# Kernel optimization log

Measured on AMD Instinct MI355X. Metric: run time of the kernel, lower is better.

## Reference

```python
import jax, jax.numpy as jnp
import numpy as np


def _log_g(x):
    # log of g(x) = where(x>=0, x+0.5, sigmoid(x)), computed stably in log-space
    return jnp.where(x >= 0, jnp.log(jax.nn.relu(x) + 0.5), -jax.nn.softplus(-x))


def _mingru_layer(h, w_hg_l, w_out_l, rms_w_l):
    # h: [B,T,H]; w_hg_l: [2*DI,H]; w_out_l: [H,DI]; rms_w_l: [H]
    hg = jnp.einsum('bth,dh->btd', h, w_hg_l)          # [B,T,2*DI]
    hidden, gate = jnp.split(hg, 2, axis=-1)            # each [B,T,DI]
    log_coeffs = -jax.nn.softplus(gate)                 # log a_t
    log_values = -jax.nn.softplus(-gate) + _log_g(hidden)  # log(z_t * g(h~_t))
    # Heinsen log-space associative scan (prev_hidden = 0, contributes nothing)
    a_star = jnp.cumsum(log_coeffs, axis=1)
    log_h = a_star + jax.lax.cumlogsumexp(log_values - a_star, axis=1)
    out = jnp.exp(log_h)                                # [B,T,DI]
    out = jnp.einsum('btd,hd->bth', out, w_out_l) + h   # proj_out + residual
    eps = jnp.finfo(out.dtype).eps
    out = out * jax.lax.rsqrt(jnp.mean(out * out, axis=-1, keepdims=True) + eps)
    return out * rms_w_l


def setup_inputs() -> dict:
    key = jax.random.key(0)
    ks = jax.random.split(key, 6)
    B, T, OBS, H, DI, L, A = 32, 1024, 512, 512, 1024, 2, 16
    s = 0.05  # weight scale keeps softplus/exp chain well-conditioned
    return {
        'x': jax.random.normal(ks[0], (B, T, OBS), jnp.float32),
        'enc_w': s * jax.random.normal(ks[1], (H, OBS), jnp.float32),
        'enc_b': jnp.zeros((H,), jnp.float32),
        'w_hg': s * jax.random.normal(ks[2], (L, 2 * DI, H), jnp.float32),
        'w_out': s * jax.random.normal(ks[3], (L, H, DI), jnp.float32),
        'rms_w': jnp.ones((L, H), jnp.float32),
        'dec_w': s * jax.random.normal(ks[4], (A, H), jnp.float32),
        'dec_b': jnp.zeros((A,), jnp.float32),
        'val_w': s * jax.random.normal(ks[5], (1, H), jnp.float32),
        'val_b': jnp.zeros((1,), jnp.float32),
    }


def reference(x, enc_w, enc_b, w_hg, w_out, rms_w, dec_w, dec_b, val_w, val_b):
    B, T, _ = x.shape
    # encoder: Linear + exact gelu
    h = jax.nn.gelu(jnp.einsum('bto,ho->bth', x, enc_w) + enc_b, approximate=False)
    for l in range(w_hg.shape[0]):
        h = _mingru_layer(h, w_hg[l], w_out[l], rms_w[l])
    flat = h.reshape(B * T, -1)
    logits = flat @ dec_w.T + dec_b                     # [B*T, A]
    values = (flat @ val_w.T + val_b).reshape(B, T)
    return logits, values
```

## Files before the change

### kernel.cpp

```cpp
#include <hip/hip_runtime.h>
#include <math.h>

#define MROWS 32768
#define T_LEN 1024

typedef __attribute__((ext_vector_type(8))) short bf16x8;
typedef __attribute__((ext_vector_type(4))) float f32x4;

__device__ __forceinline__ unsigned short f2bf(float f) {
  union { float f; unsigned u; } x; x.f = f;
  unsigned r = x.u + 0x7fffu + ((x.u >> 16) & 1u);
  return (unsigned short)(r >> 16);
}
__device__ __forceinline__ float bf2f(unsigned short u) {
  union { unsigned u; float f; } x; x.u = ((unsigned)u) << 16; return x.f;
}

__device__ __forceinline__ void gload_lds16(const void* g, void* l) {
  __builtin_amdgcn_global_load_lds(
      (const __attribute__((address_space(1))) void*)g,
      (__attribute__((address_space(3))) void*)l, 16, 0, 0);
}

__device__ __forceinline__ float sigm_neg(float x) {
  return __builtin_amdgcn_rcpf(1.0f + __expf(x));
}

#define VMCNT2 asm volatile("s_waitcnt vmcnt(2)" ::: "memory")
#define VMCNT0 asm volatile("s_waitcnt vmcnt(0)" ::: "memory")
#define LGKM0 do { asm volatile("s_waitcnt lgkmcnt(0)" ::: "memory"); \
                   __builtin_amdgcn_sched_barrier(0); } while (0)
#define BAR __builtin_amdgcn_s_barrier()

template<int MODE>
__global__ __launch_bounds__(256, 2)
void gemm_bt(const unsigned short* __restrict__ A, int lda,
             const unsigned short* __restrict__ B,
             int N, int K,
             const float* __restrict__ bias,
             const unsigned short* res,
             unsigned short* outb)
{
  __shared__ __align__(16) unsigned short sA[128 * 64];
  __shared__ __align__(16) unsigned short sB[128 * 64];
  const int tid  = threadIdx.x;
  const int wave = tid >> 6, lane = tid & 63;
  const int lid = blockIdx.x;
  const int swz = (lid & 7) * ((int)gridDim.x >> 3) + (lid >> 3);
  const int m0 = (swz >> 2) * 128;
  const int n0 = (swz & 3) * 128;
  const int srow   = lane >> 3;
  const int sslotb = ((lane & 7) ^ srow) * 16;
  const int wm = wave & 1, wn = wave >> 1;
  const int r16 = lane & 15, q = lane >> 4;

  f32x4 acc[4][4];
#pragma unroll
  for (int i = 0; i < 4; i++)
#pragma unroll
    for (int j = 0; j < 4; j++)
#pragma unroll
      for (int e = 0; e < 4; e++) acc[i][j][e] = 0.0f;

  const char* Ab = (const char*)A;
  const char* Bb = (const char*)B;
  char* sAb = (char*)sA;
  char* sBb = (char*)sB;

  for (int kt = 0; kt < K; kt += 64) {
#pragma unroll
    for (int i = 0; i < 4; i++) {
      const int j = wave * 4 + i;
      const int row = j * 8 + srow;
      gload_lds16(Ab + ((size_t)(m0 + row) * lda + kt) * 2 + sslotb, sAb + j * 1024);
      gload_lds16(Bb + ((size_t)(n0 + row) * K   + kt) * 2 + sslotb, sBb + j * 1024);
    }
    __syncthreads();
#pragma unroll
    for (int kh = 0; kh < 2; kh++) {
      bf16x8 af[4], bfr[4];
#pragma unroll
      for (int mt = 0; mt < 4; mt++) {
        const int row = wm * 64 + mt * 16 + r16;
        af[mt] = *(const bf16x8*)(sAb + row * 128 + ((((kh << 2) | q) ^ (row & 7)) * 16));
      }
#pragma unroll
      for (int nt = 0; nt < 4; nt++) {
        const int row = wn * 64 + nt * 16 + r16;
        bfr[nt] = *(const bf16x8*)(sBb + row * 128 + ((((kh << 2) | q) ^ (row & 7)) * 16));
      }
#pragma unroll
      for (int mt = 0; mt < 4; mt++)
#pragma unroll
        for (int nt = 0; nt < 4; nt++)
          acc[mt][nt] = __builtin_amdgcn_mfma_f32_16x16x32_bf16(af[mt], bfr[nt], acc[mt][nt], 0, 0, 0);
    }
    __syncthreads();
  }

#pragma unroll
  for (int mt = 0; mt < 4; mt++) {
#pragma unroll
    for (int nt = 0; nt < 4; nt++) {
#pragma unroll
      for (int r = 0; r < 4; r++) {
        const int m = m0 + wm * 64 + mt * 16 + q * 4 + r;
        const int n = n0 + wn * 64 + nt * 16 + r16;
        const size_t idx = (size_t)m * N + n;
        float v = acc[mt][nt][r];
        if (MODE == 0) {
          v += bias[n];
          v = 0.5f * v * (1.0f + erff(v * 0.70710678118654752f));
        } else if (MODE == 2) {
          v += bf2f(res[idx]);
        }
        outb[idx] = f2bf(v);
      }
    }
  }
}

__global__ __launch_bounds__(512, 2)
void gemm_hg8(const unsigned short* __restrict__ A,
              const unsigned short* __restrict__ B,
              unsigned short* __restrict__ outb)
{
  __shared__ __align__(16) char smem[131072];
  const int tid  = threadIdx.x;
  const int wave = tid >> 6, lane = tid & 63;
  const int lid = blockIdx.x;
  const int swz = (lid & 7) * 128 + (lid >> 3);
  const int m0  = (swz >> 3) * 256;
  const int nh0 = (swz & 7) * 128;
  const int wm = wave >> 2, wn = wave & 3;
  const int r16 = lane & 15, q4 = lane >> 4;

  const int srow   = tid >> 3;
  const int sslotb = ((tid & 7) ^ (srow & 7)) * 16;
  const int sldso  = tid * 16;

  const int slot0 = ((q4)     ^ (r16 & 7)) * 16;
  const int slot1 = ((4 | q4) ^ (r16 & 7)) * 16;

  const char* Ab = (const char*)A;
  const char* Bb = (const char*)B;

  f32x4 acc[8][4];
#pragma unroll
  for (int i = 0; i < 8; i++)
#pragma unroll
    for (int j = 0; j < 4; j++)
#pragma unroll
      for (int e = 0; e < 4; e++) acc[i][j][e] = 0.0f;

  auto stage2 = [&](int u, int qp) {
    char* base = smem + (u & 1) * 65536;
    const int kt2 = u << 7;
#pragma unroll
    for (int i = 0; i < 2; ++i) {
      const int qq = qp * 2 + i;
      if (qq < 4) {
        gload_lds16(Ab + (size_t)(m0 + qq * 64 + srow) * 1024 + kt2 + sslotb,
                    base + qq * 8192 + sldso);
      } else if (qq < 6) {
        gload_lds16(Bb + (size_t)(nh0 + (qq - 4) * 64 + srow) * 1024 + kt2 + sslotb,
                    base + 32768 + (qq - 4) * 8192 + sldso);
      } else {
        gload_lds16(Bb + (size_t)(1024 + nh0 + (qq - 6) * 64 + srow) * 1024 + kt2 + sslotb,
                    base + 49152 + (qq - 6) * 8192 + sldso);
      }
    }
  };

  auto lda_frags = [&](const char* base, int kh, int mh,
                       bf16x8 af[4], bf16x8 bh[2], bf16x8 bg[2]) {
    const int slot = kh ? slot1 : slot0;
#pragma unroll
    for (int mt = 0; mt < 4; ++mt) {
      const int row = wm * 128 + mh * 64 + mt * 16 + r16;
      af[mt] = *(const bf16x8*)(base + row * 128 + slot);
    }
#pragma unroll
    for (int nt = 0; nt < 2; ++nt) {
      const int row = wn * 32 + nt * 16 + r16;
      bh[nt] = *(const bf16x8*)(base + 32768 + row * 128 + slot);
      bg[nt] = *(const bf16x8*)(base + 49152 + row * 128 + slot);
    }
  };

  auto mfma16 = [&](int mh, bf16x8 af[4], bf16x8 bh[2], bf16x8 bg[2]) {
    __builtin_amdgcn_s_setprio(1);
#pragma unroll
    for (int mt = 0; mt < 4; ++mt) {
      const int MT = mh * 4 + mt;
      acc[MT][0] = __builtin_amdgcn_mfma_f32_16x16x32_bf16(af[mt], bh[0], acc[MT][0], 0, 0, 0);
      acc[MT][1] = __builtin_amdgcn_mfma_f32_16x16x32_bf16(af[mt], bh[1], acc[MT][1], 0, 0, 0);
      acc[MT][2] = __builtin_amdgcn_mfma_f32_16x16x32_bf16(af[mt], bg[0], acc[MT][2], 0, 0, 0);
      acc[MT][3] = __builtin_amdgcn_mfma_f32_16x16x32_bf16(af[mt], bg[1], acc[MT][3], 0, 0, 0);
    }
    __builtin_amdgcn_s_setprio(0);
  };

#pragma unroll
  for (int qp = 0; qp < 4; ++qp) stage2(0, qp);
  VMCNT0; BAR;

  for (int t = 0; t < 4; ++t) {
    const int u1 = 2 * t + 1;
    const char* b0 = smem;
    const char* b1 = smem + 65536;
    bf16x8 af[4], bh[2], bg[2];
    const bool more = (t < 3);

#pragma unroll
    for (int pi = 0; pi < 4; ++pi) {
      const int kh = pi >> 1, mh = pi & 1;
      if (pi == 0) {
        stage2(u1, 0);
        VMCNT2;
        BAR;
        lda_frags(b0, kh, mh, af, bh, bg);
      } else {
        lda_frags(b0, kh, mh, af, bh, bg);
        stage2(u1, pi);
        BAR;
      }
      LGKM0;
      mfma16(mh, af, bh, bg);
      BAR;
    }

#pragma unroll
    for (int pi = 0; pi < 4; ++pi) {
      const int kh = pi >> 1, mh = pi & 1;
      if (pi == 0) {
        if (more) { stage2(u1 + 1, 0); VMCNT2; } else { VMCNT0; }
        BAR;
        lda_frags(b1, kh, mh, af, bh, bg);
      } else {
        lda_frags(b1, kh, mh, af, bh, bg);
        if (more) stage2(u1 + 1, pi);
        BAR;
      }
      LGKM0;
      mfma16(mh, af, bh, bg);
      BAR;
    }
  }

#pragma unroll
  for (int MT = 0; MT < 8; ++MT) {
#pragma unroll
    for (int nf = 0; nf < 2; ++nf) {
#pragma unroll
      for (int r = 0; r < 4; ++r) {
        const int m = m0 + wm * 128 + MT * 16 + q4 * 4 + r;
        const int d = nh0 + wn * 32 + nf * 16 + r16;
        const float vh = acc[MT][nf][r];
        const float vg = acc[MT][nf + 2][r];
        const float G = (vh >= 0.0f) ? (vh + 0.5f) : sigm_neg(-vh);
        const float a = sigm_neg(vg);
        const float b = (1.0f - a) * G;
        const size_t base = (size_t)m * 2048 + d;
        outb[base]        = f2bf(b);
        outb[base + 1024] = f2bf(a);
      }
    }
  }
}

__global__ __launch_bounds__(256)
void scan_kernel(unsigned short* hg) {
  __shared__ unsigned long long sAB[256 * 16];
  __shared__ float sA[16 * 32];
  __shared__ float sH[16 * 32];
  const int b  = blockIdx.x >> 5;
  const int dg = blockIdx.x & 31;
  const int tid = threadIdx.x;
  const int c  = tid >> 4;
  const int dp = tid & 15;
  unsigned int* base = (unsigned int*)(hg + (size_t)b * T_LEN * 2048);
  const int du = dg * 16 + dp;

  float carry = 0.0f;

  for (int seg = 0; seg < 4; ++seg) {
    const int t0 = seg * 256 + c * 16;

    float A0 = 1.0f, A1 = 1.0f, h0 = 0.0f, h1 = 0.0f;
#pragma unroll
    for (int tl = 0; tl < 16; ++tl) {
      const int t = t0 + tl;
      const unsigned bpk = base[t * 1024 + du];
      const unsigned apk = base[t * 1024 + 512 + du];
      sAB[(c * 16 + tl) * 16 + dp] =
          (unsigned long long)apk | ((unsigned long long)bpk << 32);
      const float fa0 = bf2f((unsigned short)apk), fa1 = bf2f((unsigned short)(apk >> 16));
      const float fb0 = bf2f((unsigned short)bpk), fb1 = bf2f((unsigned short)(bpk >> 16));
      A0 *= fa0; h0 = fa0 * h0 + fb0;
      A1 *= fa1; h1 = fa1 * h1 + fb1;
    }
    sA[c * 32 + 2 * dp] = A0;  sA[c * 32 + 2 * dp + 1] = A1;
    sH[c * 32 + 2 * dp] = h0;  sH[c * 32 + 2 * dp + 1] = h1;
    __syncthreads();

    if (tid < 32) {
      float hin = carry;
#pragma unroll
      for (int cc = 0; cc < 16; ++cc) {
        const float a  = sA[cc * 32 + tid];
        const float hs = sH[cc * 32 + tid];
        sA[cc * 32 + tid] = hin;
        hin = hs + a * hin;
      }
      carry = hin;
    }
    __syncthreads();

    float hh0 = sA[c * 32 + 2 * dp];
    float hh1 = sA[c * 32 + 2 * dp + 1];
#pragma unroll
    for (int tl = 0; tl < 16; ++tl) {
      const int t = t0 + tl;
      const unsigned long long ab = sAB[(c * 16 + tl) * 16 + dp];
      const float fa0 = bf2f((unsigned short)ab);
      const float fa1 = bf2f((unsigned short)(ab >> 16));
      const float fb0 = bf2f((unsigned short)(ab >> 32));
      const float fb1 = bf2f((unsigned short)(ab >> 48));
      hh0 = fa0 * hh0 + fb0;
      hh1 = fa1 * hh1 + fb1;
      base[t * 1024 + 512 + du] = (unsigned)f2bf(hh0) | ((unsigned)f2bf(hh1) << 16);
    }
    __syncthreads();
  }
}

__global__ __launch_bounds__(256)
void rms_kernel(unsigned short* __restrict__ hb, const float* __restrict__ w) {
  const int wid  = (blockIdx.x * blockDim.x + threadIdx.x) >> 6;
  const int lane = threadIdx.x & 63;
  unsigned short* row = hb + (size_t)wid * 512;
  float v[8];
  float ss = 0.0f;
#pragma unroll
  for (int j = 0; j < 8; j++) { v[j] = bf2f(row[lane + 64 * j]); ss += v[j] * v[j]; }
#pragma unroll
  for (int off = 32; off >= 1; off >>= 1) ss += __shfl_xor(ss, off, 64);
  const float r = rsqrtf(ss * (1.0f / 512.0f) + 1.1920929e-7f);
#pragma unroll
  for (int j = 0; j < 8; j++) {
    const int k = lane + 64 * j;
    row[k] = f2bf(v[j] * r * w[k]);
  }
}

__global__ __launch_bounds__(256)
void rms_dec_kernel(const unsigned short* __restrict__ hb,
                    const float* __restrict__ w,
                    const float* __restrict__ dec_w,
                    const float* __restrict__ dec_b,
                    const float* __restrict__ val_w,
                    const float* __restrict__ val_b,
                    float* __restrict__ out) {
  const int row  = (blockIdx.x * blockDim.x + threadIdx.x) >> 6;
  const int lane = threadIdx.x & 63;
  const unsigned short* hr = hb + (size_t)row * 512;
  float v[8];
  float ss = 0.0f;
#pragma unroll
  for (int j = 0; j < 8; j++) { v[j] = bf2f(hr[lane + 64 * j]); ss += v[j] * v[j]; }
#pragma unroll
  for (int off = 32; off >= 1; off >>= 1) ss += __shfl_xor(ss, off, 64);
  const float r = rsqrtf(ss * (1.0f / 512.0f) + 1.1920929e-7f);

  float acc[17];
#pragma unroll
  for (int a = 0; a < 17; a++) acc[a] = 0.0f;
#pragma unroll
  for (int j = 0; j < 8; j++) {
    const int k = lane + 64 * j;
    const float hv = v[j] * r * w[k];
#pragma unroll
    for (int a = 0; a < 16; a++) acc[a] += hv * dec_w[a * 512 + k];
    acc[16] += hv * val_w[k];
  }
#pragma unroll
  for (int a = 0; a < 17; a++) {
#pragma unroll
    for (int off = 32; off >= 1; off >>= 1) acc[a] += __shfl_xor(acc[a], off, 64);
  }
  if (lane == 0) {
    float* logits = out;
    float* values = out + (size_t)MROWS * 16;
#pragma unroll
    for (int a = 0; a < 16; a++) logits[(size_t)row * 16 + a] = acc[a] + dec_b[a];
    values[row] = acc[16] + val_b[0];
  }
}

__global__ __launch_bounds__(256)
void conv_bf16(const float* __restrict__ in, unsigned short* __restrict__ out, int n4) {
  const int i = blockIdx.x * blockDim.x + threadIdx.x;
  if (i < n4) {
    const float4 v = ((const float4*)in)[i];
    const unsigned long long pack =
        (unsigned long long)f2bf(v.x) |
        ((unsigned long long)f2bf(v.y) << 16) |
        ((unsigned long long)f2bf(v.z) << 32) |
        ((unsigned long long)f2bf(v.w) << 48);
    ((unsigned long long*)out)[i] = pack;
  }
}

extern "C" void kernel_launch(void* const* d_in, const int* in_sizes, int n_in,
                              void* d_out, int out_size, void* d_ws, size_t ws_size,
                              hipStream_t stream) {
  const float* x     = (const float*)d_in[0];
  const float* enc_w = (const float*)d_in[1];
  const float* enc_b = (const float*)d_in[2];
  const float* w_hg  = (const float*)d_in[3];
  const float* w_out = (const float*)d_in[4];
  const float* rms_w = (const float*)d_in[5];
  const float* dec_w = (const float*)d_in[6];
  const float* dec_b = (const float*)d_in[7];
  const float* val_w = (const float*)d_in[8];
  const float* val_b = (const float*)d_in[9];
  float* out = (float*)d_out;

  if (ws_size < 174587904u) return;

  char* ws = (char*)d_ws;
  unsigned short* hg   = (unsigned short*)(ws);
  unsigned short* xb   = (unsigned short*)(ws);
  unsigned short* hb   = (unsigned short*)(ws + 134217728);
  unsigned short* wenc = (unsigned short*)(ws + 167772160);
  unsigned short* whg  = wenc + 262144;
  unsigned short* wout = whg + 2097152;

  conv_bf16<<<16384, 256, 0, stream>>>(x, xb, 4194304);
  conv_bf16<<<256,   256, 0, stream>>>(enc_w, wenc, 65536);
  conv_bf16<<<2048,  256, 0, stream>>>(w_hg, whg, 524288);
  conv_bf16<<<1024,  256, 0, stream>>>(w_out, wout, 262144);

  gemm_bt<0><<<1024, 256, 0, stream>>>(xb, 512, wenc, 512, 512, enc_b, nullptr, hb);

  for (int l = 0; l < 2; ++l) {
    gemm_hg8<<<1024, 512, 0, stream>>>(hb, whg + (size_t)l * 1048576, hg);
    scan_kernel<<<1024, 256, 0, stream>>>(hg);
    gemm_bt<2><<<1024, 256, 0, stream>>>(hg + 1024, 2048, wout + (size_t)l * 524288,
                                         512, 1024, nullptr, hb, hb);
    if (l == 0) rms_kernel<<<8192, 256, 0, stream>>>(hb, rms_w);
  }

  rms_dec_kernel<<<8192, 256, 0, stream>>>(hb, rms_w + 512, dec_w, dec_b,
                                           val_w, val_b, out);
}
```

Measured before the change: 572.5 us.

## Fuse x fp32-to-bf16 conversion into encoder GEMM and load A from global

Removes the standalone conversion pass over the input x. The encoder GEMM now reads fp32 A rows straight from global memory and converts them in registers. The out-projection GEMM also reads A fragments directly from global instead of staging them in LDS, and raises its occupancy hint. The three weight conversions are merged into one launch. The trade-off is less coalesced, unstaged global reads of A (reused across the wn waves only through cache) in place of the shared-memory tiles.

```diff
diff --git a/kernel.cpp b/kernel.cpp
--- a/kernel.cpp
+++ b/kernel.cpp
@@ -20,6 +20,12 @@
   __builtin_amdgcn_global_load_lds(
       (const __attribute__((address_space(1))) void*)g,
       (__attribute__((address_space(3))) void*)l, 16, 0, 0);
+}
+
+__device__ __forceinline__ unsigned cvt_pk_bf16(float lo, float hi) {
+  unsigned r;
+  asm volatile("v_cvt_pk_bf16_f32 %0, %1, %2" : "=v"(r) : "v"(lo), "v"(hi));
+  return r;
 }
 
 __device__ __forceinline__ float sigm_neg(float x) {
@@ -32,16 +38,12 @@
                    __builtin_amdgcn_sched_barrier(0); } while (0)
 #define BAR __builtin_amdgcn_s_barrier()
 
-template<int MODE>
 __global__ __launch_bounds__(256, 2)
-void gemm_bt(const unsigned short* __restrict__ A, int lda,
-             const unsigned short* __restrict__ B,
-             int N, int K,
-             const float* __restrict__ bias,
-             const unsigned short* res,
-             unsigned short* outb)
+void gemm_enc(const float* __restrict__ A,
+              const unsigned short* __restrict__ B,
+              const float* __restrict__ bias,
+              unsigned short* __restrict__ outb)
 {
-  __shared__ __align__(16) unsigned short sA[128 * 64];
   __shared__ __align__(16) unsigned short sB[128 * 64];
   const int tid  = threadIdx.x;
   const int wave = tid >> 6, lane = tid & 63;
@@ -62,18 +64,15 @@
 #pragma unroll
       for (int e = 0; e < 4; e++) acc[i][j][e] = 0.0f;
 
-  const char* Ab = (const char*)A;
   const char* Bb = (const char*)B;
-  char* sAb = (char*)sA;
   char* sBb = (char*)sB;
 
-  for (int kt = 0; kt < K; kt += 64) {
+  for (int kt = 0; kt < 512; kt += 64) {
 #pragma unroll
     for (int i = 0; i < 4; i++) {
       const int j = wave * 4 + i;
       const int row = j * 8 + srow;
-      gload_lds16(Ab + ((size_t)(m0 + row) * lda + kt) * 2 + sslotb, sAb + j * 1024);
-      gload_lds16(Bb + ((size_t)(n0 + row) * K   + kt) * 2 + sslotb, sBb + j * 1024);
+      gload_lds16(Bb + ((size_t)(n0 + row) * 512 + kt) * 2 + sslotb, sBb + j * 1024);
     }
     __syncthreads();
 #pragma unroll
@@ -81,8 +80,16 @@
       bf16x8 af[4], bfr[4];
 #pragma unroll
       for (int mt = 0; mt < 4; mt++) {
-        const int row = wm * 64 + mt * 16 + r16;
-        af[mt] = *(const bf16x8*)(sAb + row * 128 + ((((kh << 2) | q) ^ (row & 7)) * 16));
+        const float* ar = A + (size_t)(m0 + wm * 64 + mt * 16 + r16) * 512
+                            + kt + kh * 32 + q * 8;
+        const float4 x0 = *(const float4*)ar;
+        const float4 x1 = *(const float4*)(ar + 4);
+        union { unsigned u[4]; bf16x8 v; } cv;
+        cv.u[0] = cvt_pk_bf16(x0.x, x0.y);
+        cv.u[1] = cvt_pk_bf16(x0.z, x0.w);
+        cv.u[2] = cvt_pk_bf16(x1.x, x1.y);
+        cv.u[3] = cvt_pk_bf16(x1.z, x1.w);
+        af[mt] = cv.v;
       }
 #pragma unroll
       for (int nt = 0; nt < 4; nt++) {
@@ -106,15 +113,84 @@
       for (int r = 0; r < 4; r++) {
         const int m = m0 + wm * 64 + mt * 16 + q * 4 + r;
         const int n = n0 + wn * 64 + nt * 16 + r16;
-        const size_t idx = (size_t)m * N + n;
-        float v = acc[mt][nt][r];
-        if (MODE == 0) {
-          v += bias[n];
-          v = 0.5f * v * (1.0f + erff(v * 0.70710678118654752f));
-        } else if (MODE == 2) {
-          v += bf2f(res[idx]);
-        }
-        outb[idx] = f2bf(v);
+        float v = acc[mt][nt][r] + bias[n];
+        v = 0.5f * v * (1.0f + erff(v * 0.70710678118654752f));
+        outb[(size_t)m * 512 + n] = f2bf(v);
+      }
+    }
+  }
+}
+
+__global__ __launch_bounds__(256, 4)
+void gemm_oproj(const unsigned short* __restrict__ A,
+                const unsigned short* __restrict__ B,
+                const unsigned short* __restrict__ res,
+                unsigned short* __restrict__ outb)
+{
+  __shared__ __align__(16) unsigned short sB[128 * 64];
+  const int tid  = threadIdx.x;
+  const int wave = tid >> 6, lane = tid & 63;
+  const int lid = blockIdx.x;
+  const int swz = (lid & 7) * ((int)gridDim.x >> 3) + (lid >> 3);
+  const int m0 = (swz >> 2) * 128;
+  const int n0 = (swz & 3) * 128;
+  const int srow   = lane >> 3;
+  const int sslotb = ((lane & 7) ^ srow) * 16;
+  const int wm = wave & 1, wn = wave >> 1;
+  const int r16 = lane & 15, q = lane >> 4;
+
+  f32x4 acc[4][4];
+#pragma unroll
+  for (int i = 0; i < 4; i++)
+#pragma unroll
+    for (int j = 0; j < 4; j++)
+#pragma unroll
+      for (int e = 0; e < 4; e++) acc[i][j][e] = 0.0f;
+
+  const char* Ab = (const char*)A;
+  const char* Bb = (const char*)B;
+  char* sBb = (char*)sB;
+
+  for (int kt = 0; kt < 1024; kt += 64) {
+#pragma unroll
+    for (int i = 0; i < 4; i++) {
+      const int j = wave * 4 + i;
+      const int row = j * 8 + srow;
+      gload_lds16(Bb + ((size_t)(n0 + row) * 1024 + kt) * 2 + sslotb, sBb + j * 1024);
+    }
+    __syncthreads();
+#pragma unroll
+    for (int kh = 0; kh < 2; kh++) {
+      bf16x8 af[4], bfr[4];
+#pragma unroll
+      for (int mt = 0; mt < 4; mt++) {
+        af[mt] = *(const bf16x8*)(Ab +
+            ((size_t)(m0 + wm * 64 + mt * 16 + r16) * 2048 + kt + kh * 32 + q * 8) * 2);
+      }
+#pragma unroll
+      for (int nt = 0; nt < 4; nt++) {
+        const int row = wn * 64 + nt * 16 + r16;
+        bfr[nt] = *(const bf16x8*)(sBb + row * 128 + ((((kh << 2) | q) ^ (row & 7)) * 16));
+      }
+#pragma unroll
+      for (int mt = 0; mt < 4; mt++)
+#pragma unroll
+        for (int nt = 0; nt < 4; nt++)
+          acc[mt][nt] = __builtin_amdgcn_mfma_f32_16x16x32_bf16(af[mt], bfr[nt], acc[mt][nt], 0, 0, 0);
+    }
+    __syncthreads();
+  }
+
+#pragma unroll
+  for (int mt = 0; mt < 4; mt++) {
+#pragma unroll
+    for (int nt = 0; nt < 4; nt++) {
+#pragma unroll
+      for (int r = 0; r < 4; r++) {
+        const int m = m0 + wm * 64 + mt * 16 + q * 4 + r;
+        const int n = n0 + wn * 64 + nt * 16 + r16;
+        const size_t idx = (size_t)m * 512 + n;
+        outb[idx] = f2bf(acc[mt][nt][r] + bf2f(res[idx]));
       }
     }
   }
@@ -399,17 +475,22 @@
 }
 
 __global__ __launch_bounds__(256)
-void conv_bf16(const float* __restrict__ in, unsigned short* __restrict__ out, int n4) {
-  const int i = blockIdx.x * blockDim.x + threadIdx.x;
-  if (i < n4) {
-    const float4 v = ((const float4*)in)[i];
-    const unsigned long long pack =
-        (unsigned long long)f2bf(v.x) |
-        ((unsigned long long)f2bf(v.y) << 16) |
-        ((unsigned long long)f2bf(v.z) << 32) |
-        ((unsigned long long)f2bf(v.w) << 48);
-    ((unsigned long long*)out)[i] = pack;
-  }
+void conv_w(const float* __restrict__ enc_w, const float* __restrict__ w_hg,
+            const float* __restrict__ w_out,
+            unsigned short* __restrict__ wenc, unsigned short* __restrict__ whg,
+            unsigned short* __restrict__ wout) {
+  const int i = blockIdx.x * 256 + threadIdx.x;
+  const float* src; unsigned short* dst; int off;
+  if (i < 65536)        { src = enc_w; dst = wenc; off = i; }
+  else if (i < 589824)  { src = w_hg;  dst = whg;  off = i - 65536; }
+  else                  { src = w_out; dst = wout; off = i - 589824; }
+  const float4 v = ((const float4*)src)[off];
+  const unsigned long long pack =
+      (unsigned long long)f2bf(v.x) |
+      ((unsigned long long)f2bf(v.y) << 16) |
+      ((unsigned long long)f2bf(v.z) << 32) |
+      ((unsigned long long)f2bf(v.w) << 48);
+  ((unsigned long long*)dst)[off] = pack;
 }
 
 extern "C" void kernel_launch(void* const* d_in, const int* in_sizes, int n_in,
@@ -431,24 +512,19 @@
 
   char* ws = (char*)d_ws;
   unsigned short* hg   = (unsigned short*)(ws);
-  unsigned short* xb   = (unsigned short*)(ws);
   unsigned short* hb   = (unsigned short*)(ws + 134217728);
   unsigned short* wenc = (unsigned short*)(ws + 167772160);
   unsigned short* whg  = wenc + 262144;
   unsigned short* wout = whg + 2097152;
 
-  conv_bf16<<<16384, 256, 0, stream>>>(x, xb, 4194304);
-  conv_bf16<<<256,   256, 0, stream>>>(enc_w, wenc, 65536);
-  conv_bf16<<<2048,  256, 0, stream>>>(w_hg, whg, 524288);
-  conv_bf16<<<1024,  256, 0, stream>>>(w_out, wout, 262144);
-
-  gemm_bt<0><<<1024, 256, 0, stream>>>(xb, 512, wenc, 512, 512, enc_b, nullptr, hb);
+  conv_w<<<3328, 256, 0, stream>>>(enc_w, w_hg, w_out, wenc, whg, wout);
+
+  gemm_enc<<<1024, 256, 0, stream>>>(x, wenc, enc_b, hb);
 
   for (int l = 0; l < 2; ++l) {
     gemm_hg8<<<1024, 512, 0, stream>>>(hb, whg + (size_t)l * 1048576, hg);
     scan_kernel<<<1024, 256, 0, stream>>>(hg);
-    gemm_bt<2><<<1024, 256, 0, stream>>>(hg + 1024, 2048, wout + (size_t)l * 524288,
-                                         512, 1024, nullptr, hb, hb);
+    gemm_oproj<<<1024, 256, 0, stream>>>(hg + 1024, wout + (size_t)l * 524288, hb, hb);
     if (l == 0) rms_kernel<<<8192, 256, 0, stream>>>(hb, rms_w);
   }
 
```

After: 711.0 us. 1.24x slower.
